# Kernel tuning notes

Hardware: AMD Instinct MI355X
Metric: run time of the kernel (lower is better)

The kernel has to match this reference:

```python
import jax, jax.numpy as jnp
import numpy as np

N_NODES = 100000
N_EDGES = 1600000
IN_FEATS = 128
N_HIDDEN = 128
N_CLASSES = 47


def setup_inputs() -> dict:
    key = jax.random.key(0)
    ks = jax.random.split(key, 12)
    def lin(k, fi, fo):
        s = 1.0 / np.sqrt(fi)
        return jax.random.uniform(k, (fi, fo), jnp.float32, -s, s)
    return {
        "x": jax.random.normal(ks[0], (N_NODES, IN_FEATS), jnp.float32),
        "src": jax.random.randint(ks[1], (N_EDGES,), 0, N_NODES, jnp.int32),
        "dst": jax.random.randint(ks[2], (N_EDGES,), 0, N_NODES, jnp.int32),
        "W_self0": lin(ks[3], IN_FEATS, N_HIDDEN),
        "W_neigh0": lin(ks[4], IN_FEATS, N_HIDDEN),
        "b0": jnp.zeros((N_HIDDEN,), jnp.float32),
        "W_self1": lin(ks[5], N_HIDDEN, N_HIDDEN),
        "W_neigh1": lin(ks[6], N_HIDDEN, N_HIDDEN),
        "b1": jnp.zeros((N_HIDDEN,), jnp.float32),
        "W_self2": lin(ks[7], N_HIDDEN, N_CLASSES),
        "W_neigh2": lin(ks[8], N_HIDDEN, N_CLASSES),
        "b2": jnp.zeros((N_CLASSES,), jnp.float32),
    }


def _sage_layer(h, src, dst, W_self, W_neigh, b):
    # DGL SAGEConv 'mean': fc_self(h_dst) + fc_neigh(mean of in-neighbor feats) + bias
    agg = jax.ops.segment_sum(h[src], dst, num_segments=N_NODES)  # [N, d]
    deg = jax.ops.segment_sum(jnp.ones((src.shape[0],), h.dtype), dst,
                              num_segments=N_NODES)
    h_neigh = agg / jnp.maximum(deg, 1.0)[:, None]
    return h @ W_self + h_neigh @ W_neigh + b


def reference(x, src, dst, W_self0, W_neigh0, b0, W_self1, W_neigh1, b1,
              W_self2, W_neigh2, b2):
    h = _sage_layer(x, src, dst, W_self0, W_neigh0, b0)
    h = jax.nn.relu(h)
    h = _sage_layer(h, src, dst, W_self1, W_neigh1, b1)
    h = jax.nn.relu(h)
    h = _sage_layer(h, src, dst, W_self2, W_neigh2, b2)
    return h
```

## Files before the change

### kernel.cpp

```cpp
#include <hip/hip_runtime.h>

#define NN 100000
#define NE 1600000
#define NBK 391
#define CHUNK 8192
#define NBLK ((NE + CHUNK - 1) / CHUNK)
#define MPAD 100096
#define CASTB 12500
#define PREPB (CASTB + 128 + 128 + 48)
#define GBLK 2048
#define NPW ((NN + 8191) / 8192)

using bf16x8 = __attribute__((ext_vector_type(8))) short;
using f32x4  = __attribute__((ext_vector_type(4))) float;

static __device__ __forceinline__ unsigned short f2bf(float f) {
    unsigned int u = __float_as_uint(f);
    unsigned int r = (u + 0x7FFFu + ((u >> 16) & 1u)) >> 16;
    return (unsigned short)r;
}
static __device__ __forceinline__ float lo16(unsigned int u) {
    return __uint_as_float(u << 16);
}
static __device__ __forceinline__ float hi16(unsigned int u) {
    return __uint_as_float(u & 0xFFFF0000u);
}
static __device__ __forceinline__ unsigned int pk(float lo, float hi) {
    return ((unsigned int)f2bf(hi) << 16) | (unsigned int)f2bf(lo);
}


__global__ __launch_bounds__(256) void k_hist_prep(
        const int* __restrict__ dst, int* __restrict__ ghist,
        const float4* __restrict__ x4, ushort4* __restrict__ XB4,
        const float* __restrict__ Ws0, const float* __restrict__ Wn0,
        unsigned short* __restrict__ BT0,
        const float* __restrict__ Ws1, const float* __restrict__ Wn1,
        unsigned short* __restrict__ BT1,
        const float* __restrict__ Ws2, const float* __restrict__ Wn2,
        unsigned short* __restrict__ BT2) {
    __shared__ int h[NBK];
    int bid = blockIdx.x, t = threadIdx.x;
    if (bid < NBLK) {
        for (int i = t; i < NBK; i += 256) h[i] = 0;
        __syncthreads();
        int beg = bid * CHUNK, end = min(beg + CHUNK, NE);
        for (int i = beg + t; i < end; i += 256)
            atomicAdd(&h[dst[i] >> 8], 1);
        __syncthreads();
        for (int i = t; i < NBK; i += 256) ghist[bid * NBK + i] = h[i];
        return;
    }
    int pb = bid - NBLK;
    if (pb < CASTB) {
        int i = pb * 256 + t;
        float4 v = x4[i];
        ushort4 o;
        o.x = f2bf(v.x); o.y = f2bf(v.y); o.z = f2bf(v.z); o.w = f2bf(v.w);
        XB4[i] = o;
    } else if (pb < CASTB + 128) {
        int idx = (pb - CASTB) * 256 + t;
        int k = idx >> 7, n = idx & 127;
        float v = (k < 128) ? Ws0[k * 128 + n] : Wn0[(k - 128) * 128 + n];
        BT0[n * 256 + k] = f2bf(v);
    } else if (pb < CASTB + 256) {
        int idx = (pb - CASTB - 128) * 256 + t;
        int k = idx >> 7, n = idx & 127;
        float v = (k < 128) ? Ws1[k * 128 + n] : Wn1[(k - 128) * 128 + n];
        BT1[n * 256 + k] = f2bf(v);
    } else {
        int idx = (pb - CASTB - 256) * 256 + t;
        if (idx < 96 * 128) {
            int n = idx >> 7, k = idx & 127;
            float v = 0.f;
            if (n < 48) { if (n < 47) v = Ws2[k * 47 + n]; }
            else        { int cc = n - 48; if (cc < 47) v = Wn2[k * 47 + cc]; }
            BT2[n * 128 + k] = f2bf(v);
        }
    }
}

__global__ __launch_bounds__(512) void k_basescan(const int* __restrict__ ghist,
                                                  int* __restrict__ boff,
                                                  int* __restrict__ gbase) {
    __shared__ int s[512];
    int t = threadIdx.x;
    int tot = 0;
    if (t < NBK) {
#pragma unroll 4
        for (int blk = 0; blk < NBLK; ++blk) tot += ghist[blk * NBK + t];
    }
    s[t] = tot;
    __syncthreads();
    for (int o = 1; o < 512; o <<= 1) {
        int u = (t >= o) ? s[t - o] : 0;
        __syncthreads();
        s[t] += u;
        __syncthreads();
    }
    int base = s[t] - tot;
    if (t <= NBK) boff[t] = base;
    if (t < NBK) {
        int run = base;
        for (int blk = 0; blk < NBLK; ++blk) {
            int g = ghist[blk * NBK + t];
            gbase[blk * NBK + t] = run;
            run += g;
        }
    }
}

__global__ __launch_bounds__(256) void k_scatter(const int* __restrict__ src,
                                                 const int* __restrict__ dst,
                                                 const int* __restrict__ gbase,
                                                 unsigned int* __restrict__ eb) {
    __shared__ int cur[NBK];
    int b = blockIdx.x, t = threadIdx.x;
    for (int i = t; i < NBK; i += 256) cur[i] = gbase[b * NBK + i];
    __syncthreads();
    int beg = b * CHUNK, end = min(beg + CHUNK, NE);
    for (int i = beg + t; i < end; i += 256) {
        int d = dst[i];
        int p = atomicAdd(&cur[d >> 8], 1);
        eb[p] = ((unsigned int)(d & 255) << 24) | (unsigned int)src[i];
    }
}

__global__ __launch_bounds__(256) void k_csr(const unsigned int* __restrict__ eb,
                                             const int* __restrict__ boff,
                                             int* __restrict__ rp,
                                             int* __restrict__ col) {
    __shared__ int h[256];
    __shared__ int sc[256];
    __shared__ int cur[256];
    int b = blockIdx.x, t = threadIdx.x;
    h[t] = 0;
    __syncthreads();
    int beg = boff[b], end = boff[b + 1];
    for (int e = beg + t; e < end; e += 256)
        atomicAdd(&h[eb[e] >> 24], 1);
    __syncthreads();
    int c = h[t];
    sc[t] = c;
    __syncthreads();
    for (int o = 1; o < 256; o <<= 1) {
        int v = (t >= o) ? sc[t - o] : 0;
        __syncthreads();
        sc[t] += v;
        __syncthreads();
    }
    int excl = beg + sc[t] - c;
    int node = (b << 8) + t;
    if (node < NN) rp[node] = excl;
    if (node == NN - 1) rp[NN] = NE;
    cur[t] = excl;
    __syncthreads();
    for (int e = beg + t; e < end; e += 256) {
        unsigned int p = eb[e];
        int pos = atomicAdd(&cur[p >> 24], 1);
        col[pos] = (int)(p & 0xFFFFFFu);
    }
}


__global__ __launch_bounds__(256) void k_gather128(
        const uint4* __restrict__ hb4,
        const int* __restrict__ rp, const int* __restrict__ col,
        uint4* __restrict__ hnb4) {
    int wave = blockIdx.x * 4 + (threadIdx.x >> 6);
    int lane = threadIdx.x & 63;
    int q = lane >> 4, l16 = lane & 15;
    int n0 = wave * NPW;
    int n1 = min(n0 + NPW, NN);
    for (int node = n0; node < n1; ++node) {
        int beg = rp[node], end = rp[node + 1];
        float a0 = 0.f, a1 = 0.f, a2 = 0.f, a3 = 0.f;
        float a4 = 0.f, a5 = 0.f, a6 = 0.f, a7 = 0.f;
        float b0 = 0.f, b1 = 0.f, b2 = 0.f, b3 = 0.f;
        float b4 = 0.f, b5 = 0.f, b6 = 0.f, b7 = 0.f;
        int e = beg;
        for (; e + 8 <= end; e += 8) {
            int c0 = col[e + q];
            int c1 = col[e + 4 + q];
            uint4 v0 = hb4[(size_t)c0 * 16 + l16];
            uint4 v1 = hb4[(size_t)c1 * 16 + l16];
            a0 += lo16(v0.x); a1 += hi16(v0.x); a2 += lo16(v0.y); a3 += hi16(v0.y);
            a4 += lo16(v0.z); a5 += hi16(v0.z); a6 += lo16(v0.w); a7 += hi16(v0.w);
            b0 += lo16(v1.x); b1 += hi16(v1.x); b2 += lo16(v1.y); b3 += hi16(v1.y);
            b4 += lo16(v1.z); b5 += hi16(v1.z); b6 += lo16(v1.w); b7 += hi16(v1.w);
        }
        for (; e < end; e += 4) {
            if (e + q < end) {
                uint4 v = hb4[(size_t)col[e + q] * 16 + l16];
                a0 += lo16(v.x); a1 += hi16(v.x); a2 += lo16(v.y); a3 += hi16(v.y);
                a4 += lo16(v.z); a5 += hi16(v.z); a6 += lo16(v.w); a7 += hi16(v.w);
            }
        }
        float s0 = a0 + b0, s1 = a1 + b1, s2 = a2 + b2, s3 = a3 + b3;
        float s4 = a4 + b4, s5 = a5 + b5, s6 = a6 + b6, s7 = a7 + b7;
        s0 += __shfl_xor(s0, 16); s0 += __shfl_xor(s0, 32);
        s1 += __shfl_xor(s1, 16); s1 += __shfl_xor(s1, 32);
        s2 += __shfl_xor(s2, 16); s2 += __shfl_xor(s2, 32);
        s3 += __shfl_xor(s3, 16); s3 += __shfl_xor(s3, 32);
        s4 += __shfl_xor(s4, 16); s4 += __shfl_xor(s4, 32);
        s5 += __shfl_xor(s5, 16); s5 += __shfl_xor(s5, 32);
        s6 += __shfl_xor(s6, 16); s6 += __shfl_xor(s6, 32);
        s7 += __shfl_xor(s7, 16); s7 += __shfl_xor(s7, 32);
        if (q == 0) {
            float d = (float)(end - beg);
            float inv = (d > 0.f) ? 1.0f / d : 0.0f;
            uint4 o;
            o.x = pk(s0 * inv, s1 * inv);
            o.y = pk(s2 * inv, s3 * inv);
            o.z = pk(s4 * inv, s5 * inv);
            o.w = pk(s6 * inv, s7 * inv);
            hnb4[(size_t)node * 16 + l16] = o;
        }
    }
}


__global__ __launch_bounds__(256, 2) void k_mgemm(
        const unsigned short* __restrict__ A0,
        const unsigned short* __restrict__ A1,
        const unsigned short* __restrict__ BT,
        const float* __restrict__ bias,
        unsigned short* __restrict__ outB) {
    int t = threadIdx.x;
    int lane = t & 63, wid = t >> 6;
    int wm = wid >> 1, wn = wid & 1;
    int lr = lane & 15, lg = lane >> 4;
    int row0 = blockIdx.x * 128 + wm * 64;
    int colw = wn * 64;
    f32x4 zero = {0.f, 0.f, 0.f, 0.f};
    f32x4 acc[4][4];
#pragma unroll
    for (int a = 0; a < 4; ++a)
#pragma unroll
        for (int b = 0; b < 4; ++b) acc[a][b] = zero;

#pragma unroll
    for (int p = 0; p < 2; ++p) {
        const unsigned short* A = p ? A1 : A0;
        bf16x8 bReg[4][4];
#pragma unroll
        for (int nf = 0; nf < 4; ++nf)
#pragma unroll
            for (int ks = 0; ks < 4; ++ks)
                bReg[nf][ks] = *(const bf16x8*)&BT[(size_t)(colw + nf * 16 + lr) * 256 + p * 128 + ks * 32 + lg * 8];
#pragma unroll
        for (int mf = 0; mf < 4; ++mf) {
            const unsigned short* Ar = A + (size_t)(row0 + mf * 16 + lr) * 128;
            bf16x8 aReg[4];
#pragma unroll
            for (int ks = 0; ks < 4; ++ks)
                aReg[ks] = *(const bf16x8*)&Ar[ks * 32 + lg * 8];
#pragma unroll
            for (int ks = 0; ks < 4; ++ks)
#pragma unroll
                for (int nf = 0; nf < 4; ++nf)
                    acc[mf][nf] = __builtin_amdgcn_mfma_f32_16x16x32_bf16(
                        aReg[ks], bReg[nf][ks], acc[mf][nf], 0, 0, 0);
        }
    }
    __syncthreads();
#pragma unroll
    for (int nf = 0; nf < 4; ++nf) {
        int cidx = colw + nf * 16 + lr;
        float bb = bias[cidx];
#pragma unroll
        for (int mf = 0; mf < 4; ++mf) {
#pragma unroll
            for (int j = 0; j < 4; ++j) {
                int row = row0 + mf * 16 + lg * 4 + j;
                if (row < NN) {
                    float v = fmaxf(acc[mf][nf][j] + bb, 0.f);
                    outB[(size_t)row * 128 + cidx] = f2bf(v);
                }
            }
        }
    }
}


__global__ __launch_bounds__(256, 2) void k_mgemm_l12(
        const unsigned short* __restrict__ A0,
        const unsigned short* __restrict__ A1,
        const unsigned short* __restrict__ BT,
        const float* __restrict__ bias,
        unsigned short* __restrict__ outB,
        const unsigned short* __restrict__ BT2,
        const float* __restrict__ bias2,
        float* __restrict__ S,
        unsigned short* __restrict__ TB) {
    __shared__ unsigned short hl[128][132];
    int t = threadIdx.x;
    int lane = t & 63, wid = t >> 6;
    int wm = wid >> 1, wn = wid & 1;
    int lr = lane & 15, lg = lane >> 4;
    int row0 = blockIdx.x * 128 + wm * 64;
    int colw = wn * 64;
    f32x4 zero = {0.f, 0.f, 0.f, 0.f};
    f32x4 acc[4][4];
#pragma unroll
    for (int a = 0; a < 4; ++a)
#pragma unroll
        for (int b = 0; b < 4; ++b) acc[a][b] = zero;

#pragma unroll
    for (int p = 0; p < 2; ++p) {
        const unsigned short* A = p ? A1 : A0;
        bf16x8 bReg[4][4];
#pragma unroll
        for (int nf = 0; nf < 4; ++nf)
#pragma unroll
            for (int ks = 0; ks < 4; ++ks)
                bReg[nf][ks] = *(const bf16x8*)&BT[(size_t)(colw + nf * 16 + lr) * 256 + p * 128 + ks * 32 + lg * 8];
#pragma unroll
        for (int mf = 0; mf < 4; ++mf) {
            const unsigned short* Ar = A + (size_t)(row0 + mf * 16 + lr) * 128;
            bf16x8 aReg[4];
#pragma unroll
            for (int ks = 0; ks < 4; ++ks)
                aReg[ks] = *(const bf16x8*)&Ar[ks * 32 + lg * 8];
#pragma unroll
            for (int ks = 0; ks < 4; ++ks)
#pragma unroll
                for (int nf = 0; nf < 4; ++nf)
                    acc[mf][nf] = __builtin_amdgcn_mfma_f32_16x16x32_bf16(
                        aReg[ks], bReg[nf][ks], acc[mf][nf], 0, 0, 0);
        }
    }
#pragma unroll
    for (int nf = 0; nf < 4; ++nf) {
        int cidx = colw + nf * 16 + lr;
        float bb = bias[cidx];
#pragma unroll
        for (int mf = 0; mf < 4; ++mf) {
#pragma unroll
            for (int j = 0; j < 4; ++j) {
                int lrow = wm * 64 + mf * 16 + lg * 4 + j;
                float v = fmaxf(acc[mf][nf][j] + bb, 0.f);
                unsigned short bv = f2bf(v);
                hl[lrow][cidx] = bv;
                acc[mf][nf][j] = __uint_as_float((unsigned int)bv);
            }
        }
    }
    __syncthreads();
#pragma unroll
    for (int nf = 0; nf < 4; ++nf) {
        int cidx = colw + nf * 16 + lr;
#pragma unroll
        for (int mf = 0; mf < 4; ++mf) {
#pragma unroll
            for (int j = 0; j < 4; ++j) {
                int row = row0 + mf * 16 + lg * 4 + j;
                if (row < NN)
                    outB[(size_t)row * 128 + cidx] =
                        (unsigned short)__float_as_uint(acc[mf][nf][j]);
            }
        }
    }
    int colw2 = wn * 48;
    f32x4 acc2[4][3];
#pragma unroll
    for (int a = 0; a < 4; ++a)
#pragma unroll
        for (int b = 0; b < 3; ++b) acc2[a][b] = zero;
    bf16x8 bReg2[3][4];
#pragma unroll
    for (int nf = 0; nf < 3; ++nf)
#pragma unroll
        for (int ks = 0; ks < 4; ++ks)
            bReg2[nf][ks] = *(const bf16x8*)&BT2[(size_t)(colw2 + nf * 16 + lr) * 128 + ks * 32 + lg * 8];
#pragma unroll
    for (int mf = 0; mf < 4; ++mf) {
        int ar = wm * 64 + mf * 16 + lr;
        bf16x8 aReg[4];
#pragma unroll
        for (int ks = 0; ks < 4; ++ks)
            aReg[ks] = *(const bf16x8*)&hl[ar][ks * 32 + lg * 8];
#pragma unroll
        for (int ks = 0; ks < 4; ++ks)
#pragma unroll
            for (int nf = 0; nf < 3; ++nf)
                acc2[mf][nf] = __builtin_amdgcn_mfma_f32_16x16x32_bf16(
                    aReg[ks], bReg2[nf][ks], acc2[mf][nf], 0, 0, 0);
    }
#pragma unroll
    for (int nf = 0; nf < 3; ++nf) {
        int cidx = colw2 + nf * 16 + lr;
#pragma unroll
        for (int mf = 0; mf < 4; ++mf) {
#pragma unroll
            for (int j = 0; j < 4; ++j) {
                int row = row0 + mf * 16 + lg * 4 + j;
                if (row < NN) {
                    float v = acc2[mf][nf][j];
                    if (cidx < 47)
                        S[(size_t)row * 48 + cidx] = v + bias2[cidx];
                    else if (cidx >= 48)
                        TB[(size_t)row * 64 + (cidx - 48)] = f2bf(v);
                }
            }
        }
    }
}


__global__ __launch_bounds__(256) void k_gather47(
        const uint2* __restrict__ TB2,
        const float4* __restrict__ S4,
        const int* __restrict__ rp, const int* __restrict__ col,
        float* __restrict__ out) {
    int wave = blockIdx.x * 4 + (threadIdx.x >> 6);
    int lane = threadIdx.x & 63;
    int q = lane >> 4, l16 = lane & 15;
    int n0 = wave * NPW;
    int n1 = min(n0 + NPW, NN);
    for (int node = n0; node < n1; ++node) {
        int beg = rp[node], end = rp[node + 1];
        float a0 = 0.f, a1 = 0.f, a2 = 0.f, a3 = 0.f;
        float b0 = 0.f, b1 = 0.f, b2 = 0.f, b3 = 0.f;
        int e = beg;
        for (; e + 8 <= end; e += 8) {
            int i0 = col[e + q];
            int i1 = col[e + 4 + q];
            uint2 u0 = TB2[(size_t)i0 * 16 + l16];
            uint2 u1 = TB2[(size_t)i1 * 16 + l16];
            a0 += lo16(u0.x); a1 += hi16(u0.x); a2 += lo16(u0.y); a3 += hi16(u0.y);
            b0 += lo16(u1.x); b1 += hi16(u1.x); b2 += lo16(u1.y); b3 += hi16(u1.y);
        }
        for (; e < end; e += 4) {
            if (e + q < end) {
                uint2 u = TB2[(size_t)col[e + q] * 16 + l16];
                a0 += lo16(u.x); a1 += hi16(u.x); a2 += lo16(u.y); a3 += hi16(u.y);
            }
        }
        float s0 = a0 + b0, s1 = a1 + b1, s2 = a2 + b2, s3 = a3 + b3;
        s0 += __shfl_xor(s0, 16); s0 += __shfl_xor(s0, 32);
        s1 += __shfl_xor(s1, 16); s1 += __shfl_xor(s1, 32);
        s2 += __shfl_xor(s2, 16); s2 += __shfl_xor(s2, 32);
        s3 += __shfl_xor(s3, 16); s3 += __shfl_xor(s3, 32);
        if (q == 0 && l16 < 12) {
            float d = (float)(end - beg);
            float inv = (d > 0.f) ? 1.0f / d : 0.0f;
            float4 sv = S4[(size_t)node * 12 + l16];
            int c = l16 * 4;
            out[(size_t)node * 47 + c]     = sv.x + s0 * inv;
            out[(size_t)node * 47 + c + 1] = sv.y + s1 * inv;
            out[(size_t)node * 47 + c + 2] = sv.z + s2 * inv;
            if (c + 3 < 47) out[(size_t)node * 47 + c + 3] = sv.w + s3 * inv;
        }
    }
}


static inline size_t align_up(size_t x, size_t a) { return (x + a - 1) / a * a; }

extern "C" void kernel_launch(void* const* d_in, const int* in_sizes, int n_in,
                              void* d_out, int out_size, void* d_ws, size_t ws_size,
                              hipStream_t stream) {
    const float* x   = (const float*)d_in[0];
    const int* src   = (const int*)d_in[1];
    const int* dst   = (const int*)d_in[2];
    const float* Ws0 = (const float*)d_in[3];
    const float* Wn0 = (const float*)d_in[4];
    const float* b0  = (const float*)d_in[5];
    const float* Ws1 = (const float*)d_in[6];
    const float* Wn1 = (const float*)d_in[7];
    const float* b1  = (const float*)d_in[8];
    const float* Ws2 = (const float*)d_in[9];
    const float* Wn2 = (const float*)d_in[10];
    const float* b2  = (const float*)d_in[11];
    float* out = (float*)d_out;

    char* ws = (char*)d_ws;
    size_t off = 0;
    auto alloc = [&](size_t bytes) -> void* {
        void* p = ws + off; off = align_up(off + bytes, 256); return p;
    };
    int* row_ptr = (int*)alloc((size_t)(NN + 1) * 4);
    int* boff    = (int*)alloc((size_t)(NBK + 1) * 4);
    int* gbase   = (int*)alloc((size_t)NBLK * NBK * 4);
    int* ghist   = (int*)alloc((size_t)NBLK * NBK * 4);
    int* col     = (int*)alloc((size_t)NE * 4);
    unsigned short* XB  = (unsigned short*)alloc((size_t)MPAD * 128 * 2);
    unsigned short* BT0 = (unsigned short*)alloc(128 * 256 * 2);
    unsigned short* BT1 = (unsigned short*)alloc(128 * 256 * 2);
    unsigned short* BT2 = (unsigned short*)alloc(96 * 128 * 2);
    unsigned int* HNB   = (unsigned int*)alloc((size_t)MPAD * 128 * 2);
    size_t sbytes  = (size_t)NN * 48 * 4;
    size_t tbbytes = (size_t)MPAD * 64 * 2;
    char* stb = (char*)alloc(sbytes + tbbytes);
    unsigned int* eb   = (unsigned int*)stb;
    float* S           = (float*)stb;
    unsigned short* TB = (unsigned short*)(stb + sbytes);

    k_hist_prep<<<NBLK + PREPB, 256, 0, stream>>>(
        dst, ghist, (const float4*)x, (ushort4*)XB,
        Ws0, Wn0, BT0, Ws1, Wn1, BT1, Ws2, Wn2, BT2);
    k_basescan<<<1, 512, 0, stream>>>(ghist, boff, gbase);
    k_scatter<<<NBLK, 256, 0, stream>>>(src, dst, gbase, eb);
    k_csr<<<NBK, 256, 0, stream>>>(eb, boff, row_ptr, col);

    int mgrid = MPAD / 128;

    k_gather128<<<GBLK, 256, 0, stream>>>((const uint4*)XB, row_ptr, col, (uint4*)HNB);
    k_mgemm<<<mgrid, 256, 0, stream>>>(XB, (const unsigned short*)HNB, BT0, b0, XB);
    k_gather128<<<GBLK, 256, 0, stream>>>((const uint4*)XB, row_ptr, col, (uint4*)HNB);
    k_mgemm_l12<<<mgrid, 256, 0, stream>>>(XB, (const unsigned short*)HNB, BT1, b1, XB,
                                           BT2, b2, S, TB);
    k_gather47<<<GBLK, 256, 0, stream>>>((const uint2*)TB, (const float4*)S,
                                         row_ptr, col, out);
}
```

Before: 343.8 us.

## Stage GEMM A tiles into LDS via direct global-to-LDS loads with XOR swizzle

Both dense GEMM kernels now load each 128x128 bf16 A tile cooperatively into shared memory using global_load_lds. An XOR swizzle avoids bank conflicts, and MFMA operands are read from LDS instead of each wave issuing strided global loads. The second kernel reuses the same swizzled buffer for the intermediate hidden tile and writes outB directly in the epilogue, removing the separate store pass. This adds barriers per K-phase and reduces unrolling (unroll 1 on the phase loop), which could limit overlap of loads and MFMAs.

```diff
diff --git a/kernel.cpp b/kernel.cpp
--- a/kernel.cpp
+++ b/kernel.cpp
@@ -13,6 +13,9 @@
 
 using bf16x8 = __attribute__((ext_vector_type(8))) short;
 using f32x4  = __attribute__((ext_vector_type(4))) float;
+
+typedef const __attribute__((address_space(1))) unsigned int* gas_t;
+typedef __attribute__((address_space(3))) unsigned int* las_t;
 
 static __device__ __forceinline__ unsigned short f2bf(float f) {
     unsigned int u = __float_as_uint(f);
@@ -226,11 +229,13 @@
         const unsigned short* __restrict__ BT,
         const float* __restrict__ bias,
         unsigned short* __restrict__ outB) {
+    __shared__ char sA[32768];
     int t = threadIdx.x;
     int lane = t & 63, wid = t >> 6;
     int wm = wid >> 1, wn = wid & 1;
     int lr = lane & 15, lg = lane >> 4;
-    int row0 = blockIdx.x * 128 + wm * 64;
+    int brow = blockIdx.x * 128;
+    int row0 = brow + wm * 64;
     int colw = wn * 64;
     f32x4 zero = {0.f, 0.f, 0.f, 0.f};
     f32x4 acc[4][4];
@@ -239,9 +244,18 @@
 #pragma unroll
         for (int b = 0; b < 4; ++b) acc[a][b] = zero;
 
-#pragma unroll
+#pragma unroll 1
     for (int p = 0; p < 2; ++p) {
         const unsigned short* A = p ? A1 : A0;
+#pragma unroll
+        for (int it = 0; it < 8; ++it) {
+            int rl = wid * 32 + it * 4 + (lane >> 4);
+            int ch = (lane & 15) ^ (rl & 7);
+            const char* src = (const char*)A + (size_t)(brow + rl) * 256 + ch * 16;
+            __builtin_amdgcn_global_load_lds((gas_t)src,
+                (las_t)(sA + wid * 8192 + it * 1024), 16, 0, 0);
+        }
+        __syncthreads();
         bf16x8 bReg[4][4];
 #pragma unroll
         for (int nf = 0; nf < 4; ++nf)
@@ -250,11 +264,11 @@
                 bReg[nf][ks] = *(const bf16x8*)&BT[(size_t)(colw + nf * 16 + lr) * 256 + p * 128 + ks * 32 + lg * 8];
 #pragma unroll
         for (int mf = 0; mf < 4; ++mf) {
-            const unsigned short* Ar = A + (size_t)(row0 + mf * 16 + lr) * 128;
+            int rl = wm * 64 + mf * 16 + lr;
             bf16x8 aReg[4];
 #pragma unroll
             for (int ks = 0; ks < 4; ++ks)
-                aReg[ks] = *(const bf16x8*)&Ar[ks * 32 + lg * 8];
+                aReg[ks] = *(const bf16x8*)&sA[rl * 256 + (((ks * 4 + lg) ^ (rl & 7)) << 4)];
 #pragma unroll
             for (int ks = 0; ks < 4; ++ks)
 #pragma unroll
@@ -262,8 +276,8 @@
                     acc[mf][nf] = __builtin_amdgcn_mfma_f32_16x16x32_bf16(
                         aReg[ks], bReg[nf][ks], acc[mf][nf], 0, 0, 0);
         }
-    }
-    __syncthreads();
+        __syncthreads();
+    }
 #pragma unroll
     for (int nf = 0; nf < 4; ++nf) {
         int cidx = colw + nf * 16 + lr;
@@ -293,12 +307,13 @@
         const float* __restrict__ bias2,
         float* __restrict__ S,
         unsigned short* __restrict__ TB) {
-    __shared__ unsigned short hl[128][132];
+    __shared__ char sA[32768];
     int t = threadIdx.x;
     int lane = t & 63, wid = t >> 6;
     int wm = wid >> 1, wn = wid & 1;
     int lr = lane & 15, lg = lane >> 4;
-    int row0 = blockIdx.x * 128 + wm * 64;
+    int brow = blockIdx.x * 128;
+    int row0 = brow + wm * 64;
     int colw = wn * 64;
     f32x4 zero = {0.f, 0.f, 0.f, 0.f};
     f32x4 acc[4][4];
@@ -307,9 +322,18 @@
 #pragma unroll
         for (int b = 0; b < 4; ++b) acc[a][b] = zero;
 
-#pragma unroll
+#pragma unroll 1
     for (int p = 0; p < 2; ++p) {
         const unsigned short* A = p ? A1 : A0;
+#pragma unroll
+        for (int it = 0; it < 8; ++it) {
+            int rl = wid * 32 + it * 4 + (lane >> 4);
+            int ch = (lane & 15) ^ (rl & 7);
+            const char* src = (const char*)A + (size_t)(brow + rl) * 256 + ch * 16;
+            __builtin_amdgcn_global_load_lds((gas_t)src,
+                (las_t)(sA + wid * 8192 + it * 1024), 16, 0, 0);
+        }
+        __syncthreads();
         bf16x8 bReg[4][4];
 #pragma unroll
         for (int nf = 0; nf < 4; ++nf)
@@ -318,11 +342,11 @@
                 bReg[nf][ks] = *(const bf16x8*)&BT[(size_t)(colw + nf * 16 + lr) * 256 + p * 128 + ks * 32 + lg * 8];
 #pragma unroll
         for (int mf = 0; mf < 4; ++mf) {
-            const unsigned short* Ar = A + (size_t)(row0 + mf * 16 + lr) * 128;
+            int rl = wm * 64 + mf * 16 + lr;
             bf16x8 aReg[4];
 #pragma unroll
             for (int ks = 0; ks < 4; ++ks)
-                aReg[ks] = *(const bf16x8*)&Ar[ks * 32 + lg * 8];
+                aReg[ks] = *(const bf16x8*)&sA[rl * 256 + (((ks * 4 + lg) ^ (rl & 7)) << 4)];
 #pragma unroll
             for (int ks = 0; ks < 4; ++ks)
 #pragma unroll
@@ -330,6 +354,7 @@
                     acc[mf][nf] = __builtin_amdgcn_mfma_f32_16x16x32_bf16(
                         aReg[ks], bReg[nf][ks], acc[mf][nf], 0, 0, 0);
         }
+        __syncthreads();
     }
 #pragma unroll
     for (int nf = 0; nf < 4; ++nf) {
@@ -342,26 +367,13 @@
                 int lrow = wm * 64 + mf * 16 + lg * 4 + j;
                 float v = fmaxf(acc[mf][nf][j] + bb, 0.f);
                 unsigned short bv = f2bf(v);
-                hl[lrow][cidx] = bv;
-                acc[mf][nf][j] = __uint_as_float((unsigned int)bv);
+                *(unsigned short*)&sA[lrow * 256 + ((((cidx >> 3) ^ (lrow & 7)) << 4)) + (cidx & 7) * 2] = bv;
+                int row = brow + lrow;
+                if (row < NN) outB[(size_t)row * 128 + cidx] = bv;
             }
         }
     }
     __syncthreads();
-#pragma unroll
-    for (int nf = 0; nf < 4; ++nf) {
-        int cidx = colw + nf * 16 + lr;
-#pragma unroll
-        for (int mf = 0; mf < 4; ++mf) {
-#pragma unroll
-            for (int j = 0; j < 4; ++j) {
-                int row = row0 + mf * 16 + lg * 4 + j;
-                if (row < NN)
-                    outB[(size_t)row * 128 + cidx] =
-                        (unsigned short)__float_as_uint(acc[mf][nf][j]);
-            }
-        }
-    }
     int colw2 = wn * 48;
     f32x4 acc2[4][3];
 #pragma unroll
@@ -376,11 +388,11 @@
             bReg2[nf][ks] = *(const bf16x8*)&BT2[(size_t)(colw2 + nf * 16 + lr) * 128 + ks * 32 + lg * 8];
 #pragma unroll
     for (int mf = 0; mf < 4; ++mf) {
-        int ar = wm * 64 + mf * 16 + lr;
+        int rl = wm * 64 + mf * 16 + lr;
         bf16x8 aReg[4];
 #pragma unroll
         for (int ks = 0; ks < 4; ++ks)
-            aReg[ks] = *(const bf16x8*)&hl[ar][ks * 32 + lg * 8];
+            aReg[ks] = *(const bf16x8*)&sA[rl * 256 + (((ks * 4 + lg) ^ (rl & 7)) << 4)];
 #pragma unroll
         for (int ks = 0; ks < 4; ++ks)
 #pragma unroll
@@ -395,7 +407,7 @@
         for (int mf = 0; mf < 4; ++mf) {
 #pragma unroll
             for (int j = 0; j < 4; ++j) {
-                int row = row0 + mf * 16 + lg * 4 + j;
+                int row = brow + wm * 64 + mf * 16 + lg * 4 + j;
                 if (row < NN) {
                     float v = acc2[mf][nf][j];
                     if (cidx < 47)
```

After: 333.7 us. 1.03x faster.
